# Performance work log

Hardware: AMD Instinct MI355X
Metric: run time of the kernel (lower is better)

Reference implementation:

```python
import jax, jax.numpy as jnp
import numpy as np

D_MODEL = 1024
H = 16
D_K = D_MODEL // H
WINDOW = 256
NEG = -1.0e9


def setup_inputs() -> dict:
    key = jax.random.key(0)
    ks = jax.random.split(key, 12)
    B, S = 1, 4096
    scale = 1.0 / np.sqrt(D_MODEL)
    inp = {
        'q': jax.random.normal(ks[0], (B, S, D_MODEL), dtype=jnp.float32),
        'k': jax.random.normal(ks[1], (B, S, D_MODEL), dtype=jnp.float32),
        'v': jax.random.normal(ks[2], (B, S, D_MODEL), dtype=jnp.float32),
        'w_q': jax.random.normal(ks[3], (D_MODEL, D_MODEL), dtype=jnp.float32) * scale,
        'b_q': jnp.zeros((D_MODEL,), dtype=jnp.float32),
        'w_k': jax.random.normal(ks[4], (D_MODEL, D_MODEL), dtype=jnp.float32) * scale,
        'b_k': jnp.zeros((D_MODEL,), dtype=jnp.float32),
        'w_v': jax.random.normal(ks[5], (D_MODEL, D_MODEL), dtype=jnp.float32) * scale,
        'b_v': jnp.zeros((D_MODEL,), dtype=jnp.float32),
        'w_o': jax.random.normal(ks[6], (D_MODEL, D_MODEL), dtype=jnp.float32) * scale,
        'b_o': jnp.zeros((D_MODEL,), dtype=jnp.float32),
    }
    return inp


def _local_mask(seq_len: int, window_size: int) -> jnp.ndarray:
    left = (window_size - 1) // 2
    right = window_size - 1 - left
    row = jnp.arange(seq_len)[:, None]
    col = jnp.arange(seq_len)[None, :]
    return (col >= row - left) & (col <= row + right)  # [S, S] bool


def reference(q, k, v, w_q, b_q, w_k, b_k, w_v, b_v, w_o, b_o):
    B, Sq, _ = q.shape
    Sk = k.shape[1]
    # projections (torch Linear: x @ W.T + b) -> [B, h, S, d_k]
    query = (q @ w_q.T + b_q).reshape(B, Sq, H, D_K).transpose(0, 2, 1, 3)
    key = (k @ w_k.T + b_k).reshape(B, Sk, H, D_K).transpose(0, 2, 1, 3)
    value = (v @ w_v.T + b_v).reshape(B, Sk, H, D_K).transpose(0, 2, 1, 3)

    scores = jnp.einsum('bhqd,bhkd->bhqk', query, key) / jnp.sqrt(
        jnp.asarray(D_K, dtype=query.dtype))
    if Sq == Sk:
        mask = _local_mask(Sq, WINDOW)  # [S, S]
        scores = jnp.where(mask[None, None], scores, jnp.asarray(NEG, scores.dtype))
    attn = jax.nn.softmax(scores, axis=-1)
    x = jnp.einsum('bhqk,bhkd->bhqd', attn, value)
    x = x.transpose(0, 2, 1, 3).reshape(B, Sq, D_MODEL)
    return x @ w_o.T + b_o
```

## Files before the change

kernel.cpp:

```cpp
#include <hip/hip_runtime.h>

#define SEQ 4096
#define DM 1024
#define NH 16
#define DK 64
#define NTW 3

typedef _Float16 half8 __attribute__((ext_vector_type(8)));
typedef _Float16 half4v __attribute__((ext_vector_type(4)));
typedef float f32x4 __attribute__((ext_vector_type(4)));

#define MFMA16(a, b, c) __builtin_amdgcn_mfma_f32_16x16x32_f16((a), (b), (c), 0, 0, 0)

__global__ void cvt_all(const float* __restrict__ q, const float* __restrict__ k,
                        const float* __restrict__ v, const float* __restrict__ wq,
                        const float* __restrict__ wk, const float* __restrict__ wv,
                        const float* __restrict__ wo, _Float16* __restrict__ qh,
                        _Float16* __restrict__ kh, _Float16* __restrict__ vh,
                        _Float16* __restrict__ wqh, _Float16* __restrict__ wkh,
                        _Float16* __restrict__ wvh, _Float16* __restrict__ woh) {
    int z = blockIdx.y;
    const float* src;
    _Float16* dst;
    int n;
    switch (z) {
    case 0: src = q;  dst = qh;  n = SEQ * DM; break;
    case 1: src = k;  dst = kh;  n = SEQ * DM; break;
    case 2: src = v;  dst = vh;  n = SEQ * DM; break;
    case 3: src = wq; dst = wqh; n = DM * DM;  break;
    case 4: src = wk; dst = wkh; n = DM * DM;  break;
    case 5: src = wv; dst = wvh; n = DM * DM;  break;
    default: src = wo; dst = woh; n = DM * DM; break;
    }
    int idx = (blockIdx.x * 256 + threadIdx.x) * 4;
    if (idx >= n) return;
    float4 f = *(const float4*)(src + idx);
    half4v h;
    h[0] = (_Float16)f.x; h[1] = (_Float16)f.y; h[2] = (_Float16)f.z; h[3] = (_Float16)f.w;
    *(half4v*)(dst + idx) = h;
}

template <int MT>
__device__ __forceinline__ void gemm_core(const _Float16* __restrict__ A,
                                          const _Float16* __restrict__ B,
                                          const float* __restrict__ bias,
                                          void* __restrict__ Cout, int mode, float scale) {
    const int K = DM;
    const int N = DM;
    constexpr int MI = MT / 32;
    constexpr int ACH = MT / 64;
    __shared__ _Float16 As[MT * 32];
    __shared__ _Float16 Bs[128 * 32];
    int tid = threadIdx.x;
    int wave = tid >> 6, lane = tid & 63;
    int quad = lane >> 4, l16 = lane & 15;
    int m0 = blockIdx.x * MT;
    int n0 = blockIdx.y * 128;
    int wr = (wave >> 1) * (MT / 2);
    int wc = (wave & 1) * 64;
    f32x4 acc[MI][4] = {};

    for (int k0 = 0; k0 < K; k0 += 32) {
#pragma unroll
        for (int j = 0; j < ACH; ++j) {
            int c = j * 256 + tid;
            int row = c >> 2, cc = c & 3;
            const _Float16* ga = A + (size_t)(m0 + row) * K + k0 + cc * 8;
            __builtin_amdgcn_global_load_lds(
                (const __attribute__((address_space(1))) void*)ga,
                (__attribute__((address_space(3))) void*)(As + j * 2048 + wave * 512), 16, 0, 0);
        }
#pragma unroll
        for (int j = 0; j < 2; ++j) {
            int c = j * 256 + tid;
            int row = c >> 2, cc = c & 3;
            const _Float16* gb = B + (size_t)(n0 + row) * K + k0 + cc * 8;
            __builtin_amdgcn_global_load_lds(
                (const __attribute__((address_space(1))) void*)gb,
                (__attribute__((address_space(3))) void*)(Bs + j * 2048 + wave * 512), 16, 0, 0);
        }
        __syncthreads();
        half8 af[MI], bf[4];
#pragma unroll
        for (int mi = 0; mi < MI; ++mi)
            af[mi] = *(const half8*)&As[(wr + mi * 16 + l16) * 32 + quad * 8];
#pragma unroll
        for (int ni = 0; ni < 4; ++ni)
            bf[ni] = *(const half8*)&Bs[(wc + ni * 16 + l16) * 32 + quad * 8];
#pragma unroll
        for (int mi = 0; mi < MI; ++mi)
#pragma unroll
            for (int ni = 0; ni < 4; ++ni)
                acc[mi][ni] = MFMA16(af[mi], bf[ni], acc[mi][ni]);
        __syncthreads();
    }

    float bs[4];
#pragma unroll
    for (int ni = 0; ni < 4; ++ni) bs[ni] = bias[n0 + wc + ni * 16 + l16];

    if (mode == 0) {
        _Float16* C = (_Float16*)Cout;
#pragma unroll
        for (int mi = 0; mi < MI; ++mi)
#pragma unroll
            for (int ni = 0; ni < 4; ++ni) {
                int m = m0 + wr + mi * 16 + quad * 4;
                int n = n0 + wc + ni * 16 + l16;
#pragma unroll
                for (int r = 0; r < 4; ++r)
                    C[(size_t)(m + r) * N + n] = (_Float16)((acc[mi][ni][r] + bs[ni]) * scale);
            }
    } else if (mode == 1) {
        _Float16* C = (_Float16*)Cout;
#pragma unroll
        for (int mi = 0; mi < MI; ++mi)
#pragma unroll
            for (int ni = 0; ni < 4; ++ni) {
                int m = m0 + wr + mi * 16 + quad * 4;
                int n = n0 + wc + ni * 16 + l16;
                half4v p;
#pragma unroll
                for (int r = 0; r < 4; ++r) p[r] = (_Float16)(acc[mi][ni][r] + bs[ni]);
                *(half4v*)(C + (size_t)n * SEQ + m) = p;
            }
    } else {
        float* C = (float*)Cout;
#pragma unroll
        for (int mi = 0; mi < MI; ++mi)
#pragma unroll
            for (int ni = 0; ni < 4; ++ni) {
                int m = m0 + wr + mi * 16 + quad * 4;
                int n = n0 + wc + ni * 16 + l16;
#pragma unroll
                for (int r = 0; r < 4; ++r)
                    C[(size_t)(m + r) * N + n] = acc[mi][ni][r] + bs[ni];
            }
    }
}

__global__ void gemm_qkv(const _Float16* __restrict__ qh, const _Float16* __restrict__ kh,
                         const _Float16* __restrict__ vh, const _Float16* __restrict__ wqh,
                         const _Float16* __restrict__ wkh, const _Float16* __restrict__ wvh,
                         const float* __restrict__ bq, const float* __restrict__ bk,
                         const float* __restrict__ bv, _Float16* __restrict__ Qo,
                         _Float16* __restrict__ Ko, _Float16* __restrict__ Vt) {
    int z = blockIdx.z;
    const _Float16 *A, *B;
    const float* bias;
    void* C;
    int mode;
    float scale;
    if (z == 0) { A = qh; B = wqh; bias = bq; C = Qo; mode = 0; scale = 0.125f; }
    else if (z == 1) { A = kh; B = wkh; bias = bk; C = Ko; mode = 0; scale = 1.0f; }
    else { A = vh; B = wvh; bias = bv; C = Vt; mode = 1; scale = 1.0f; }
    gemm_core<128>(A, B, bias, C, mode, scale);
}

__global__ void gemm_out(const _Float16* __restrict__ Xh, const _Float16* __restrict__ woh,
                         const float* __restrict__ bo, float* __restrict__ out) {
    gemm_core<64>(Xh, woh, bo, out, 2, 1.0f);
}

__global__ void __launch_bounds__(256, 2) attn_kernel(const _Float16* __restrict__ Q,
                                                      const _Float16* __restrict__ K,
                                                      const _Float16* __restrict__ Vt,
                                                      _Float16* __restrict__ X) {
    __shared__ char smem[512 + 4 * 64 * 20 * 4];
    _Float16(*Pl)[2][16][40] = (_Float16(*)[2][16][40])smem;
    float2* MS = (float2*)smem;
    float* Ob = (float*)(smem + 512);

    int tid = threadIdx.x;
    int wave = tid >> 6, lane = tid & 63;
    int quad = lane >> 4, l16 = lane & 15;
    int h = blockIdx.y;
    int q0 = blockIdx.x * 16;

    const _Float16* Qp = Q + (size_t)(q0 + l16) * DM + h * DK + quad * 8;
    half8 aq0 = *(const half8*)(Qp);
    half8 aq1 = *(const half8*)(Qp + 32);

    int kstart = (q0 > 127) ? ((q0 - 127) & ~31) : 0;

    f32x4 s[NTW][2];
#pragma unroll
    for (int j = 0; j < NTW; ++j) {
        int kt = kstart + (wave + 4 * j) * 32;
#pragma unroll
        for (int cf = 0; cf < 2; ++cf) {
            int krow = kt + cf * 16 + l16;
            int kc = krow < SEQ ? krow : SEQ - 1;
            const _Float16* Kp = K + (size_t)kc * DM + h * DK + quad * 8;
            half8 b0 = *(const half8*)(Kp);
            half8 b1 = *(const half8*)(Kp + 32);
            f32x4 z = {};
            z = MFMA16(aq0, b0, z);
            z = MFMA16(aq1, b1, z);
            s[j][cf] = z;
        }
    }

#pragma unroll
    for (int j = 0; j < NTW; ++j)
#pragma unroll
        for (int cf = 0; cf < 2; ++cf) {
            int key = kstart + (wave + 4 * j) * 32 + cf * 16 + l16;
#pragma unroll
            for (int r = 0; r < 4; ++r) {
                int row = q0 + quad * 4 + r;
                bool valid = (key >= row - 127) && (key <= row + 128) && (key < SEQ);
                if (!valid) s[j][cf][r] = -1e30f;
            }
        }
    float rowM[4];
#pragma unroll
    for (int r = 0; r < 4; ++r) {
        float m = -1e30f;
#pragma unroll
        for (int j = 0; j < NTW; ++j) m = fmaxf(m, fmaxf(s[j][0][r], s[j][1][r]));
#pragma unroll
        for (int off = 1; off < 16; off <<= 1) m = fmaxf(m, __shfl_xor(m, off));
        rowM[r] = m;
    }

    f32x4 o[4] = {};
    float sum[4] = {0.f, 0.f, 0.f, 0.f};
#pragma unroll
    for (int j = 0; j < NTW; ++j) {
        int vcol = kstart + (wave + 4 * j) * 32 + quad * 8;
        int vc = vcol < SEQ ? vcol : 0;
#pragma unroll
        for (int r = 0; r < 4; ++r) {
            float p0 = __expf(s[j][0][r] - rowM[r]);
            float p1 = __expf(s[j][1][r] - rowM[r]);
            Pl[wave][j & 1][quad * 4 + r][l16] = (_Float16)p0;
            Pl[wave][j & 1][quad * 4 + r][l16 + 16] = (_Float16)p1;
            sum[r] += p0 + p1;
        }
        half8 ap = *(const half8*)&Pl[wave][j & 1][l16][quad * 8];
#pragma unroll
        for (int ni = 0; ni < 4; ++ni) {
            const _Float16* Vp = Vt + (size_t)(h * DK + ni * 16 + l16) * SEQ + vc;
            half8 bv = *(const half8*)(Vp);
            o[ni] = MFMA16(ap, bv, o[ni]);
        }
    }
#pragma unroll
    for (int r = 0; r < 4; ++r) {
        float sm = sum[r];
#pragma unroll
        for (int off = 1; off < 16; off <<= 1) sm += __shfl_xor(sm, off);
        sum[r] = sm;
    }

    __syncthreads();
    if (l16 == 0) {
#pragma unroll
        for (int r = 0; r < 4; ++r)
            MS[wave * 16 + quad * 4 + r] = make_float2(rowM[r], sum[r]);
    }
#pragma unroll
    for (int ni = 0; ni < 4; ++ni)
        *(f32x4*)&Ob[(wave * 64 + lane) * 20 + ni * 4] = o[ni];
    __syncthreads();

    int niq = wave;
    float f[4][4], rinv[4];
#pragma unroll
    for (int r = 0; r < 4; ++r) {
        float2 msv[4];
        float M = -1e30f;
#pragma unroll
        for (int w = 0; w < 4; ++w) {
            msv[w] = MS[w * 16 + quad * 4 + r];
            M = fmaxf(M, msv[w].x);
        }
        float S = 0.f;
#pragma unroll
        for (int w = 0; w < 4; ++w) {
            f[w][r] = __expf(msv[w].x - M);
            S += f[w][r] * msv[w].y;
        }
        rinv[r] = 1.0f / S;
    }
    f32x4 acc = {};
#pragma unroll
    for (int w = 0; w < 4; ++w) {
        f32x4 ov = *(const f32x4*)&Ob[(w * 64 + lane) * 20 + niq * 4];
#pragma unroll
        for (int r = 0; r < 4; ++r) acc[r] += f[w][r] * ov[r];
    }
#pragma unroll
    for (int r = 0; r < 4; ++r) {
        int m = q0 + quad * 4 + r;
        X[(size_t)m * DM + h * DK + niq * 16 + l16] = (_Float16)(acc[r] * rinv[r]);
    }
}

extern "C" void kernel_launch(void* const* d_in, const int* in_sizes, int n_in, void* d_out,
                              int out_size, void* d_ws, size_t ws_size, hipStream_t stream) {
    const float* q  = (const float*)d_in[0];
    const float* k  = (const float*)d_in[1];
    const float* v  = (const float*)d_in[2];
    const float* wq = (const float*)d_in[3];
    const float* bq = (const float*)d_in[4];
    const float* wk = (const float*)d_in[5];
    const float* bk = (const float*)d_in[6];
    const float* wv = (const float*)d_in[7];
    const float* bv = (const float*)d_in[8];
    const float* wo = (const float*)d_in[9];
    const float* bo = (const float*)d_in[10];

    const size_t SZ_T = (size_t)SEQ * DM * sizeof(_Float16);
    const size_t SZ_W = (size_t)DM * DM * sizeof(_Float16);
    char* p = (char*)d_ws;
    _Float16* qh  = (_Float16*)(p);
    _Float16* kh  = (_Float16*)(p + SZ_T);
    _Float16* vh  = (_Float16*)(p + 2 * SZ_T);
    _Float16* wqh = (_Float16*)(p + 3 * SZ_T);
    _Float16* wkh = (_Float16*)(p + 3 * SZ_T + SZ_W);
    _Float16* wvh = (_Float16*)(p + 3 * SZ_T + 2 * SZ_W);
    _Float16* woh = (_Float16*)(p + 3 * SZ_T + 3 * SZ_W);
    _Float16* Qo  = (_Float16*)(p + 3 * SZ_T + 4 * SZ_W);
    _Float16* Ko  = (_Float16*)(p + 4 * SZ_T + 4 * SZ_W);
    _Float16* Vt  = (_Float16*)(p + 5 * SZ_T + 4 * SZ_W);
    _Float16* Xh  = qh;

    cvt_all<<<dim3(4096, 7), 256, 0, stream>>>(q, k, v, wq, wk, wv, wo, qh, kh, vh, wqh, wkh,
                                               wvh, woh);
    gemm_qkv<<<dim3(32, 8, 3), 256, 0, stream>>>(qh, kh, vh, wqh, wkh, wvh, bq, bk, bv, Qo, Ko,
                                                 Vt);
    attn_kernel<<<dim3(SEQ / 16, NH), 256, 0, stream>>>(Qo, Ko, Vt, Xh);
    gemm_out<<<dim3(64, 8), 256, 0, stream>>>(Xh, woh, bo, (float*)d_out);
}
```

Measured before the change: 228.5 us.

## Double-buffer GEMM loads, shrink GEMM tiles, swizzle attention blocks, pad LDS

Replaces the shared GEMM core with a double-buffered loop. It issues the next K-slice's global-to-LDS loads before computing the current slice and uses one barrier per iteration instead of two. Tiles shrink to 64x128 for the QKV GEMM and 64x64 for the output GEMM, which doubles the block count for better occupancy and wave balance. The attention kernel remaps block indices to interleave query tiles, and pads the per-wave output LDS stride from 20 to 21 floats to reduce bank conflicts. The odd stride leaves the 16-byte vector LDS accesses misaligned, which may split them or be unsafe.

```diff
diff --git a/kernel.cpp b/kernel.cpp
--- a/kernel.cpp
+++ b/kernel.cpp
@@ -11,6 +11,9 @@
 typedef float f32x4 __attribute__((ext_vector_type(4)));
 
 #define MFMA16(a, b, c) __builtin_amdgcn_mfma_f32_16x16x32_f16((a), (b), (c), 0, 0, 0)
+#define GLOAD_LDS(g, l)                                                              \
+    __builtin_amdgcn_global_load_lds((const __attribute__((address_space(1))) void*)(g), \
+                                     (__attribute__((address_space(3))) void*)(l), 16, 0, 0)
 
 __global__ void cvt_all(const float* __restrict__ q, const float* __restrict__ k,
                         const float* __restrict__ v, const float* __restrict__ wq,
@@ -40,81 +43,105 @@
     *(half4v*)(dst + idx) = h;
 }
 
-template <int MT>
-__device__ __forceinline__ void gemm_core(const _Float16* __restrict__ A,
-                                          const _Float16* __restrict__ B,
-                                          const float* __restrict__ bias,
-                                          void* __restrict__ Cout, int mode, float scale) {
-    const int K = DM;
-    const int N = DM;
-    constexpr int MI = MT / 32;
-    constexpr int ACH = MT / 64;
-    __shared__ _Float16 As[MT * 32];
-    __shared__ _Float16 Bs[128 * 32];
-    int tid = threadIdx.x;
-    int wave = tid >> 6, lane = tid & 63;
-    int quad = lane >> 4, l16 = lane & 15;
-    int m0 = blockIdx.x * MT;
+template <int NT>
+__device__ __forceinline__ void gemm64_loop(const _Float16* __restrict__ A,
+                                            const _Float16* __restrict__ B, int m0, int n0,
+                                            _Float16* As, _Float16* Bs, f32x4 (*acc)[NT / 32]) {
+    constexpr int NBC = NT / 64;
+    constexpr int NR = NT / 32;
+    const int tid = threadIdx.x;
+    const int wave = tid >> 6, lane = tid & 63;
+    const int quad = lane >> 4, l16 = lane & 15;
+    const int wr = (wave >> 1) * 32;
+    const int wc = (wave & 1) * (NT / 2);
+    const int srow = tid >> 2, scol = (tid & 3) * 8;
+    const _Float16* ga = A + (size_t)(m0 + srow) * DM + scol;
+    const _Float16* gb = B + (size_t)(n0 + srow) * DM + scol;
+    const int dofs = tid * 8;
+
+    GLOAD_LDS(ga, As + dofs);
+#pragma unroll
+    for (int j = 0; j < NBC; ++j) GLOAD_LDS(gb + j * 64 * DM, Bs + j * 2048 + dofs);
+
+    int pb = 0;
+    for (int k0 = 0; k0 < DM; k0 += 32) {
+        __builtin_amdgcn_s_waitcnt(0x0F70);
+        __builtin_amdgcn_s_barrier();
+        const int nb = pb ^ 1;
+        if (k0 + 32 < DM) {
+            GLOAD_LDS(ga + k0 + 32, As + nb * 2048 + dofs);
+#pragma unroll
+            for (int j = 0; j < NBC; ++j)
+                GLOAD_LDS(gb + k0 + 32 + j * 64 * DM, Bs + (nb * NBC + j) * 2048 + dofs);
+        }
+        const _Float16* as = As + pb * 2048;
+        const _Float16* bs = Bs + pb * NBC * 2048;
+        half8 af[2], bf[NR];
+#pragma unroll
+        for (int mi = 0; mi < 2; ++mi)
+            af[mi] = *(const half8*)&as[(wr + mi * 16 + l16) * 32 + quad * 8];
+#pragma unroll
+        for (int ni = 0; ni < NR; ++ni)
+            bf[ni] = *(const half8*)&bs[(wc + ni * 16 + l16) * 32 + quad * 8];
+#pragma unroll
+        for (int mi = 0; mi < 2; ++mi)
+#pragma unroll
+            for (int ni = 0; ni < NR; ++ni) acc[mi][ni] = MFMA16(af[mi], bf[ni], acc[mi][ni]);
+        pb = nb;
+    }
+}
+
+__global__ void __launch_bounds__(256) gemm_qkv(const _Float16* __restrict__ qh,
+                                                const _Float16* __restrict__ kh,
+                                                const _Float16* __restrict__ vh,
+                                                const _Float16* __restrict__ wqh,
+                                                const _Float16* __restrict__ wkh,
+                                                const _Float16* __restrict__ wvh,
+                                                const float* __restrict__ bq,
+                                                const float* __restrict__ bk,
+                                                const float* __restrict__ bv,
+                                                _Float16* __restrict__ Qo,
+                                                _Float16* __restrict__ Ko,
+                                                _Float16* __restrict__ Vt) {
+    __shared__ _Float16 As[2 * 2048];
+    __shared__ _Float16 Bs[2 * 2 * 2048];
+    int z = blockIdx.z;
+    const _Float16 *A, *B;
+    const float* bias;
+    float scale;
+    if (z == 0) { A = qh; B = wqh; bias = bq; scale = 0.125f; }
+    else if (z == 1) { A = kh; B = wkh; bias = bk; scale = 1.0f; }
+    else { A = vh; B = wvh; bias = bv; scale = 1.0f; }
+
+    int m0 = blockIdx.x * 64;
     int n0 = blockIdx.y * 128;
-    int wr = (wave >> 1) * (MT / 2);
-    int wc = (wave & 1) * 64;
-    f32x4 acc[MI][4] = {};
-
-    for (int k0 = 0; k0 < K; k0 += 32) {
-#pragma unroll
-        for (int j = 0; j < ACH; ++j) {
-            int c = j * 256 + tid;
-            int row = c >> 2, cc = c & 3;
-            const _Float16* ga = A + (size_t)(m0 + row) * K + k0 + cc * 8;
-            __builtin_amdgcn_global_load_lds(
-                (const __attribute__((address_space(1))) void*)ga,
-                (__attribute__((address_space(3))) void*)(As + j * 2048 + wave * 512), 16, 0, 0);
-        }
-#pragma unroll
-        for (int j = 0; j < 2; ++j) {
-            int c = j * 256 + tid;
-            int row = c >> 2, cc = c & 3;
-            const _Float16* gb = B + (size_t)(n0 + row) * K + k0 + cc * 8;
-            __builtin_amdgcn_global_load_lds(
-                (const __attribute__((address_space(1))) void*)gb,
-                (__attribute__((address_space(3))) void*)(Bs + j * 2048 + wave * 512), 16, 0, 0);
-        }
-        __syncthreads();
-        half8 af[MI], bf[4];
-#pragma unroll
-        for (int mi = 0; mi < MI; ++mi)
-            af[mi] = *(const half8*)&As[(wr + mi * 16 + l16) * 32 + quad * 8];
-#pragma unroll
-        for (int ni = 0; ni < 4; ++ni)
-            bf[ni] = *(const half8*)&Bs[(wc + ni * 16 + l16) * 32 + quad * 8];
-#pragma unroll
-        for (int mi = 0; mi < MI; ++mi)
-#pragma unroll
-            for (int ni = 0; ni < 4; ++ni)
-                acc[mi][ni] = MFMA16(af[mi], bf[ni], acc[mi][ni]);
-        __syncthreads();
-    }
-
+    f32x4 acc[2][4] = {};
+    gemm64_loop<128>(A, B, m0, n0, As, Bs, acc);
+
+    const int tid = threadIdx.x;
+    const int wave = tid >> 6, lane = tid & 63;
+    const int quad = lane >> 4, l16 = lane & 15;
+    const int wr = (wave >> 1) * 32;
+    const int wc = (wave & 1) * 64;
     float bs[4];
 #pragma unroll
     for (int ni = 0; ni < 4; ++ni) bs[ni] = bias[n0 + wc + ni * 16 + l16];
 
-    if (mode == 0) {
-        _Float16* C = (_Float16*)Cout;
-#pragma unroll
-        for (int mi = 0; mi < MI; ++mi)
+    if (z < 2) {
+        _Float16* C = (z == 0) ? Qo : Ko;
+#pragma unroll
+        for (int mi = 0; mi < 2; ++mi)
 #pragma unroll
             for (int ni = 0; ni < 4; ++ni) {
                 int m = m0 + wr + mi * 16 + quad * 4;
                 int n = n0 + wc + ni * 16 + l16;
 #pragma unroll
                 for (int r = 0; r < 4; ++r)
-                    C[(size_t)(m + r) * N + n] = (_Float16)((acc[mi][ni][r] + bs[ni]) * scale);
+                    C[(size_t)(m + r) * DM + n] = (_Float16)((acc[mi][ni][r] + bs[ni]) * scale);
             }
-    } else if (mode == 1) {
-        _Float16* C = (_Float16*)Cout;
-#pragma unroll
-        for (int mi = 0; mi < MI; ++mi)
+    } else {
+#pragma unroll
+        for (int mi = 0; mi < 2; ++mi)
 #pragma unroll
             for (int ni = 0; ni < 4; ++ni) {
                 int m = m0 + wr + mi * 16 + quad * 4;
@@ -122,51 +149,44 @@
                 half4v p;
 #pragma unroll
                 for (int r = 0; r < 4; ++r) p[r] = (_Float16)(acc[mi][ni][r] + bs[ni]);
-                *(half4v*)(C + (size_t)n * SEQ + m) = p;
+                *(half4v*)(Vt + (size_t)n * SEQ + m) = p;
             }
-    } else {
-        float* C = (float*)Cout;
-#pragma unroll
-        for (int mi = 0; mi < MI; ++mi)
-#pragma unroll
-            for (int ni = 0; ni < 4; ++ni) {
-                int m = m0 + wr + mi * 16 + quad * 4;
-                int n = n0 + wc + ni * 16 + l16;
-#pragma unroll
-                for (int r = 0; r < 4; ++r)
-                    C[(size_t)(m + r) * N + n] = acc[mi][ni][r] + bs[ni];
-            }
-    }
-}
-
-__global__ void gemm_qkv(const _Float16* __restrict__ qh, const _Float16* __restrict__ kh,
-                         const _Float16* __restrict__ vh, const _Float16* __restrict__ wqh,
-                         const _Float16* __restrict__ wkh, const _Float16* __restrict__ wvh,
-                         const float* __restrict__ bq, const float* __restrict__ bk,
-                         const float* __restrict__ bv, _Float16* __restrict__ Qo,
-                         _Float16* __restrict__ Ko, _Float16* __restrict__ Vt) {
-    int z = blockIdx.z;
-    const _Float16 *A, *B;
-    const float* bias;
-    void* C;
-    int mode;
-    float scale;
-    if (z == 0) { A = qh; B = wqh; bias = bq; C = Qo; mode = 0; scale = 0.125f; }
-    else if (z == 1) { A = kh; B = wkh; bias = bk; C = Ko; mode = 0; scale = 1.0f; }
-    else { A = vh; B = wvh; bias = bv; C = Vt; mode = 1; scale = 1.0f; }
-    gemm_core<128>(A, B, bias, C, mode, scale);
-}
-
-__global__ void gemm_out(const _Float16* __restrict__ Xh, const _Float16* __restrict__ woh,
-                         const float* __restrict__ bo, float* __restrict__ out) {
-    gemm_core<64>(Xh, woh, bo, out, 2, 1.0f);
+    }
+}
+
+__global__ void __launch_bounds__(256) gemm_out(const _Float16* __restrict__ Xh,
+                                                const _Float16* __restrict__ woh,
+                                                const float* __restrict__ bo,
+                                                float* __restrict__ out) {
+    __shared__ _Float16 As[2 * 2048];
+    __shared__ _Float16 Bs[2 * 2048];
+    int m0 = blockIdx.x * 64;
+    int n0 = blockIdx.y * 64;
+    f32x4 acc[2][2] = {};
+    gemm64_loop<64>(Xh, woh, m0, n0, As, Bs, acc);
+
+    const int tid = threadIdx.x;
+    const int wave = tid >> 6, lane = tid & 63;
+    const int quad = lane >> 4, l16 = lane & 15;
+    const int wr = (wave >> 1) * 32;
+    const int wc = (wave & 1) * 32;
+#pragma unroll
+    for (int mi = 0; mi < 2; ++mi)
+#pragma unroll
+        for (int ni = 0; ni < 2; ++ni) {
+            int m = m0 + wr + mi * 16 + quad * 4;
+            int n = n0 + wc + ni * 16 + l16;
+            float b = bo[n];
+#pragma unroll
+            for (int r = 0; r < 4; ++r) out[(size_t)(m + r) * DM + n] = acc[mi][ni][r] + b;
+        }
 }
 
 __global__ void __launch_bounds__(256, 2) attn_kernel(const _Float16* __restrict__ Q,
                                                       const _Float16* __restrict__ K,
                                                       const _Float16* __restrict__ Vt,
                                                       _Float16* __restrict__ X) {
-    __shared__ char smem[512 + 4 * 64 * 20 * 4];
+    __shared__ char smem[512 + 4 * 64 * 21 * 4];
     _Float16(*Pl)[2][16][40] = (_Float16(*)[2][16][40])smem;
     float2* MS = (float2*)smem;
     float* Ob = (float*)(smem + 512);
@@ -175,7 +195,8 @@
     int wave = tid >> 6, lane = tid & 63;
     int quad = lane >> 4, l16 = lane & 15;
     int h = blockIdx.y;
-    int q0 = blockIdx.x * 16;
+    int bx = ((blockIdx.x & 7) << 5) + (blockIdx.x >> 3);
+    int q0 = bx * 16;
 
     const _Float16* Qp = Q + (size_t)(q0 + l16) * DM + h * DK + quad * 8;
     half8 aq0 = *(const half8*)(Qp);
@@ -262,7 +283,7 @@
     }
 #pragma unroll
     for (int ni = 0; ni < 4; ++ni)
-        *(f32x4*)&Ob[(wave * 64 + lane) * 20 + ni * 4] = o[ni];
+        *(f32x4*)&Ob[(wave * 64 + lane) * 21 + ni * 4] = o[ni];
     __syncthreads();
 
     int niq = wave;
@@ -287,7 +308,7 @@
     f32x4 acc = {};
 #pragma unroll
     for (int w = 0; w < 4; ++w) {
-        f32x4 ov = *(const f32x4*)&Ob[(w * 64 + lane) * 20 + niq * 4];
+        f32x4 ov = *(const f32x4*)&Ob[(w * 64 + lane) * 21 + niq * 4];
 #pragma unroll
         for (int r = 0; r < 4; ++r) acc[r] += f[w][r] * ov[r];
     }
@@ -329,8 +350,8 @@
 
     cvt_all<<<dim3(4096, 7), 256, 0, stream>>>(q, k, v, wq, wk, wv, wo, qh, kh, vh, wqh, wkh,
                                                wvh, woh);
-    gemm_qkv<<<dim3(32, 8, 3), 256, 0, stream>>>(qh, kh, vh, wqh, wkh, wvh, bq, bk, bv, Qo, Ko,
+    gemm_qkv<<<dim3(64, 8, 3), 256, 0, stream>>>(qh, kh, vh, wqh, wkh, wvh, bq, bk, bv, Qo, Ko,
                                                  Vt);
     attn_kernel<<<dim3(SEQ / 16, NH), 256, 0, stream>>>(Qo, Ko, Vt, Xh);
-    gemm_out<<<dim3(64, 8), 256, 0, stream>>>(Xh, woh, bo, (float*)d_out);
-}
+    gemm_out<<<dim3(64, 16), 256, 0, stream>>>(Xh, woh, bo, (float*)d_out);
+}
```

Result: slower. 247.8 us (+8.4%).
